# Kernel optimization log

Hardware: AMD Instinct MI355X
Metric: run time of the kernel (lower is better)

The kernel has to match this reference:

```python
import jax, jax.numpy as jnp
import numpy as np

B, D, N = 16, 512, 8192
K = 2048  # codebook_size


def setup_inputs() -> dict:
    key = jax.random.key(0)
    k1, k2 = jax.random.split(key)
    x = jax.random.normal(k1, (B, D, N), dtype=jnp.float32)
    embed = jax.random.normal(k2, (K, D), dtype=jnp.float32)  # codebook [K, D]
    return {"x": x, "embed": embed}


def reference(x, embed):
    # x: [B, D, N] -> [B, N, D] -> flatten to [B*N, D]
    xt = jnp.transpose(x, (0, 2, 1))
    flat = xt.reshape(-1, xt.shape[-1])  # [B*N, D]
    x2 = jnp.sum(flat * flat, axis=1, keepdims=True)            # [B*N, 1]
    e2 = jnp.sum(embed * embed, axis=1)[None, :]                 # [1, K]
    dist = -(x2 - 2.0 * (flat @ embed.T) + e2)                   # [B*N, K]
    embed_ind = jnp.argmax(dist, axis=-1)                        # [B*N]
    embed_ind = embed_ind.reshape(B, N)                          # [B, N]
    quantize = embed[embed_ind]                                  # [B, N, D]
    quantize = jnp.transpose(quantize, (0, 2, 1))                # [B, D, N]
    return (quantize, embed_ind)
```

## Files before the change

### kernel.cpp

```cpp
#include <hip/hip_runtime.h>
#include <math.h>
#include <stdint.h>


constexpr int B = 16, D = 512, N = 8192, K = 2048;

typedef __attribute__((ext_vector_type(8)))  short   short8;
typedef __attribute__((ext_vector_type(16))) float   floatx16;

typedef const __attribute__((address_space(1))) uint32_t* gas1_t;
typedef __attribute__((address_space(3)))       uint32_t* las3_t;

__device__ __forceinline__ void async_ld16(const void* g, void* lds) {
  __builtin_amdgcn_global_load_lds((gas1_t)g, (las3_t)lds, 16, 0, 0);
}

__device__ __forceinline__ uint32_t rne_hi(float a) {
  uint32_t u = __float_as_uint(a);
  return (u + 0x7fffu + ((u >> 16) & 1u)) & 0xffff0000u;
}

__device__ __forceinline__ void split2(float a, float b, uint32_t& hi, uint32_t& lo) {
  uint32_t ha = rne_hi(a), hb = rne_hi(b);
  float ra = a - __uint_as_float(ha);
  float rb = b - __uint_as_float(hb);
  hi = (ha >> 16) | hb;
  uint32_t la = rne_hi(ra), lb = rne_hi(rb);
  lo = (la >> 16) | lb;
}

__global__ __launch_bounds__(256) void e2_kernel(const float* __restrict__ embed,
                                                 float* __restrict__ e2) {
  int k = blockIdx.x * 4 + (threadIdx.x >> 6);
  int lane = threadIdx.x & 63;
  const float* row = embed + (size_t)k * D;
  float s = 0.f;
  #pragma unroll
  for (int d = 0; d < D; d += 64) {
    float v = row[d + lane];
    s = fmaf(v, v, s);
  }
  #pragma unroll
  for (int off = 32; off; off >>= 1) s += __shfl_down(s, off, 64);
  if (lane == 0) e2[k] = s;
}

__global__ __launch_bounds__(256) void split_x(const float* __restrict__ x,
                                               ushort* __restrict__ xhi,
                                               ushort* __restrict__ xlo) {
  const int n = blockIdx.x * 256 + threadIdx.x;
  const int g = blockIdx.y;
  const int b = blockIdx.z;
  const float* src = x + (size_t)(b * 64 + g) * 8 * N + n;
  union { ushort u[8]; short8 s; } H, L;
  #pragma unroll
  for (int r = 0; r < 8; ++r) {
    float a = src[(size_t)r * N];
    uint32_t ha = rne_hi(a);
    float ra = a - __uint_as_float(ha);
    uint32_t la = rne_hi(ra);
    H.u[r] = (ushort)(ha >> 16);
    L.u[r] = (ushort)(la >> 16);
  }
  size_t o = ((size_t)(b * 64 + g) * N + n) * 8;
  *(short8*)&xhi[o] = H.s;
  *(short8*)&xlo[o] = L.s;
}

__global__ __launch_bounds__(256) void split_e(const float* __restrict__ embed,
                                               ushort* __restrict__ ehi,
                                               ushort* __restrict__ elo) {
  const int kt = blockIdx.x, dt = blockIdx.y;
  const int t = threadIdx.x;
  const int f4 = t & 15;
  const int cr = t >> 4;
  const int run = f4 >> 1, half = f4 & 1;
  const size_t tileo = (size_t)(kt * 8 + dt) * 8192;
  const float* eb = embed + (size_t)(kt * 128) * D + dt * 64;
  #pragma unroll
  for (int p = 0; p < 8; ++p) {
    int c = p * 16 + cr;
    const float4 v = *(const float4*)(eb + (size_t)c * D + f4 * 4);
    uint32_t h0, l0, h1, l1;
    split2(v.x, v.y, h0, l0);
    split2(v.z, v.w, h1, l1);
    size_t off = tileo + (size_t)(run * 128 + c) * 8 + half * 4;
    *(uint2*)&ehi[off] = make_uint2(h0, h1);
    *(uint2*)&elo[off] = make_uint2(l0, l1);
  }
}

__global__ __launch_bounds__(256, 2) void vq_mfma2(const ushort* __restrict__ xhi,
                                                   const ushort* __restrict__ xlo,
                                                   const ushort* __restrict__ ehi,
                                                   const ushort* __restrict__ elo,
                                                   const float* __restrict__ e2g,
                                                   const float* __restrict__ embed,
                                                   float* __restrict__ out) {
  __shared__ ushort Xh[8192], Xl[8192];
  __shared__ ushort Eh[8192], El[8192];
  __shared__ float redV[512];
  __shared__ int   redI[512];
  __shared__ int   fIdx[128];

  const int t    = threadIdx.x;
  const int lane = t & 63;
  const int wid  = t >> 6;
  const int wm   = wid & 1;
  const int wn   = wid >> 1;
  const int l31  = lane & 31;
  const int lh   = lane >> 5;

  const int b  = blockIdx.y;
  const int n0 = blockIdx.x * 128;

  float bestV[2] = {-3.402823466e38f, -3.402823466e38f};
  int   bestI[2] = {0, 0};

  for (int kt = 0; kt < K / 128; ++kt) {
    floatx16 acc[2][2];
    #pragma unroll
    for (int mt = 0; mt < 2; ++mt)
      #pragma unroll
      for (int nt = 0; nt < 2; ++nt)
        #pragma unroll
        for (int i = 0; i < 16; ++i) acc[mt][nt][i] = 0.f;

    for (int dt = 0; dt < D / 64; ++dt) {
      #pragma unroll
      for (int i = 0; i < 2; ++i) {
        int gg = wid * 2 + i;
        const ushort* sh = xhi + ((size_t)(b * 64 + dt * 8 + gg) * N + n0) * 8;
        const ushort* sl = xlo + ((size_t)(b * 64 + dt * 8 + gg) * N + n0) * 8;
        #pragma unroll
        for (int j = 0; j < 2; ++j) {
          async_ld16(sh + (size_t)j * 512 + lane * 8, &Xh[gg * 1024 + j * 512]);
          async_ld16(sl + (size_t)j * 512 + lane * 8, &Xl[gg * 1024 + j * 512]);
        }
      }
      {
        const size_t tileo = (size_t)(kt * 8 + dt) * 8192;
        const ushort* sh = ehi + tileo + wid * 2048;
        const ushort* sl = elo + tileo + wid * 2048;
        #pragma unroll
        for (int i = 0; i < 4; ++i) {
          async_ld16(sh + i * 512 + lane * 8, &Eh[wid * 2048 + i * 512]);
          async_ld16(sl + i * 512 + lane * 8, &El[wid * 2048 + i * 512]);
        }
      }
      __syncthreads();

      #pragma unroll
      for (int ks = 0; ks < 4; ++ks) {
        const int run = ks * 2 + lh;
        short8 ah[2], al[2];
        #pragma unroll
        for (int mt = 0; mt < 2; ++mt) {
          int c = wm * 64 + mt * 32 + l31;
          int eo = (run * 128 + c) * 8;
          ah[mt] = *(const short8*)&Eh[eo];
          al[mt] = *(const short8*)&El[eo];
        }
        short8 bh[2], bl[2];
        #pragma unroll
        for (int nt = 0; nt < 2; ++nt) {
          int n = wn * 64 + nt * 32 + l31;
          int xo = (run * 128 + n) * 8;
          bh[nt] = *(const short8*)&Xh[xo];
          bl[nt] = *(const short8*)&Xl[xo];
        }
        #pragma unroll
        for (int mt = 0; mt < 2; ++mt)
          #pragma unroll
          for (int nt = 0; nt < 2; ++nt) {
            acc[mt][nt] = __builtin_amdgcn_mfma_f32_32x32x16_bf16(
                ah[mt], bh[nt], acc[mt][nt], 0, 0, 0);
            acc[mt][nt] = __builtin_amdgcn_mfma_f32_32x32x16_bf16(
                ah[mt], bl[nt], acc[mt][nt], 0, 0, 0);
            acc[mt][nt] = __builtin_amdgcn_mfma_f32_32x32x16_bf16(
                al[mt], bh[nt], acc[mt][nt], 0, 0, 0);
          }
      }
      __syncthreads();
    }

    #pragma unroll
    for (int mt = 0; mt < 2; ++mt) {
      #pragma unroll
      for (int r = 0; r < 16; ++r) {
        int row  = (r & 3) + 8 * (r >> 2) + 4 * lh;
        int code = kt * 128 + wm * 64 + mt * 32 + row;
        float ek = e2g[code];
        #pragma unroll
        for (int nt = 0; nt < 2; ++nt) {
          float s = 2.0f * acc[mt][nt][r] - ek;
          if (s > bestV[nt]) { bestV[nt] = s; bestI[nt] = code; }
        }
      }
    }
  }

  __syncthreads();
  #pragma unroll
  for (int nt = 0; nt < 2; ++nt) {
    int n = wn * 64 + nt * 32 + l31;
    int slot = lh + 2 * wm;
    redV[n * 4 + slot] = bestV[nt];
    redI[n * 4 + slot] = bestI[nt];
  }
  __syncthreads();
  if (t < 128) {
    float bv = redV[t * 4]; int bi = redI[t * 4];
    #pragma unroll
    for (int s = 1; s < 4; ++s) {
      float v = redV[t * 4 + s]; int ii = redI[t * 4 + s];
      if (v > bv || (v == bv && ii < bi)) { bv = v; bi = ii; }
    }
    fIdx[t] = bi;
    out[(size_t)B * D * N + (size_t)b * N + n0 + t] = (float)bi;
  }
  __syncthreads();

  {
    int n = t & 127;
    int code = fIdx[n];
    const float* erow = embed + (size_t)code * D;
    float* ob = out + (size_t)b * D * N + n0 + n;
    for (int d = (t >> 7); d < D; d += 2) {
      ob[(size_t)d * N] = erow[d];
    }
  }
}

__global__ __launch_bounds__(256, 2) void vq_mfma(const float* __restrict__ x,
                                                  const float* __restrict__ embed,
                                                  const float* __restrict__ e2g,
                                                  float* __restrict__ out) {
  __shared__ float    Xraw[64 * 128];
  __shared__ uint16_t Ehi[128 * 64];
  __shared__ uint16_t Elo[128 * 64];

  const int t    = threadIdx.x;
  const int lane = t & 63;
  const int wid  = t >> 6;
  const int wm   = wid & 1;
  const int wn   = wid >> 1;
  const int l31  = lane & 31;
  const int lh   = lane >> 5;

  const int b  = blockIdx.y;
  const int n0 = blockIdx.x * 128;
  const float* xb = x + (size_t)b * D * N + n0;

  float bestV[2] = {-3.402823466e38f, -3.402823466e38f};
  int   bestI[2] = {0, 0};

  for (int kt = 0; kt < K / 128; ++kt) {
    floatx16 acc[2][2];
    #pragma unroll
    for (int mt = 0; mt < 2; ++mt)
      #pragma unroll
      for (int nt = 0; nt < 2; ++nt)
        #pragma unroll
        for (int i = 0; i < 16; ++i) acc[mt][nt][i] = 0.f;

    for (int dt = 0; dt < D / 64; ++dt) {
      {
        const float* g0 = xb + (size_t)(dt * 64 + wid * 16 + lh) * N + l31 * 4;
        #pragma unroll
        for (int i = 0; i < 8; ++i) {
          async_ld16(g0 + (size_t)(i * 2) * N, &Xraw[(wid * 16 + i * 2) * 128]);
        }
      }
      {
        const float* eb = embed + (size_t)(kt * 128) * D + dt * 64;
        const int f4 = t & 15;
        const int cr = t >> 4;
        #pragma unroll
        for (int p = 0; p < 8; ++p) {
          int c = p * 16 + cr;
          const float4 v = *(const float4*)(eb + (size_t)c * D + f4 * 4);
          uint32_t h0, l0, h1, l1;
          split2(v.x, v.y, h0, l0);
          split2(v.z, v.w, h1, l1);
          int run = f4 >> 1, half = f4 & 1;
          int off = ((run ^ (c & 7)) * 8 + half * 4);
          *(uint2*)&Ehi[c * 64 + off] = make_uint2(h0, h1);
          *(uint2*)&Elo[c * 64 + off] = make_uint2(l0, l1);
        }
      }
      __syncthreads();

      #pragma unroll
      for (int ks = 0; ks < 4; ++ks) {
        short8 ahi[2], alo[2];
        #pragma unroll
        for (int mt = 0; mt < 2; ++mt) {
          int c = wm * 64 + mt * 32 + l31;
          int run = ks * 2 + lh;
          int off = (run ^ (c & 7)) * 8;
          ahi[mt] = *(const short8*)&Ehi[c * 64 + off];
          alo[mt] = *(const short8*)&Elo[c * 64 + off];
        }
        short8 bhi[2], blo[2];
        #pragma unroll
        for (int nt = 0; nt < 2; ++nt) {
          int n = wn * 64 + nt * 32 + l31;
          int kb = ks * 16 + lh * 8;
          float r0 = Xraw[(kb + 0) * 128 + n];
          float r1 = Xraw[(kb + 1) * 128 + n];
          float r2 = Xraw[(kb + 2) * 128 + n];
          float r3 = Xraw[(kb + 3) * 128 + n];
          float r4 = Xraw[(kb + 4) * 128 + n];
          float r5 = Xraw[(kb + 5) * 128 + n];
          float r6 = Xraw[(kb + 6) * 128 + n];
          float r7 = Xraw[(kb + 7) * 128 + n];
          union { short8 s; uint32_t u[4]; } Bh, Bl;
          split2(r0, r1, Bh.u[0], Bl.u[0]);
          split2(r2, r3, Bh.u[1], Bl.u[1]);
          split2(r4, r5, Bh.u[2], Bl.u[2]);
          split2(r6, r7, Bh.u[3], Bl.u[3]);
          bhi[nt] = Bh.s; blo[nt] = Bl.s;
        }
        #pragma unroll
        for (int mt = 0; mt < 2; ++mt)
          #pragma unroll
          for (int nt = 0; nt < 2; ++nt) {
            acc[mt][nt] = __builtin_amdgcn_mfma_f32_32x32x16_bf16(
                ahi[mt], bhi[nt], acc[mt][nt], 0, 0, 0);
            acc[mt][nt] = __builtin_amdgcn_mfma_f32_32x32x16_bf16(
                ahi[mt], blo[nt], acc[mt][nt], 0, 0, 0);
            acc[mt][nt] = __builtin_amdgcn_mfma_f32_32x32x16_bf16(
                alo[mt], bhi[nt], acc[mt][nt], 0, 0, 0);
          }
      }
      __syncthreads();
    }

    #pragma unroll
    for (int mt = 0; mt < 2; ++mt) {
      #pragma unroll
      for (int r = 0; r < 16; ++r) {
        int row  = (r & 3) + 8 * (r >> 2) + 4 * lh;
        int code = kt * 128 + wm * 64 + mt * 32 + row;
        float ek = e2g[code];
        #pragma unroll
        for (int nt = 0; nt < 2; ++nt) {
          float s = 2.0f * acc[mt][nt][r] - ek;
          if (s > bestV[nt]) { bestV[nt] = s; bestI[nt] = code; }
        }
      }
    }
  }

  __syncthreads();
  float* redV = Xraw;
  int*   redI = (int*)(Xraw + 512);
  int*   fIdx = (int*)(Xraw + 1024);

  #pragma unroll
  for (int nt = 0; nt < 2; ++nt) {
    int n = wn * 64 + nt * 32 + l31;
    int slot = lh + 2 * wm;
    redV[n * 4 + slot] = bestV[nt];
    redI[n * 4 + slot] = bestI[nt];
  }
  __syncthreads();
  if (t < 128) {
    float bv = redV[t * 4]; int bi = redI[t * 4];
    #pragma unroll
    for (int s = 1; s < 4; ++s) {
      float v = redV[t * 4 + s]; int ii = redI[t * 4 + s];
      if (v > bv || (v == bv && ii < bi)) { bv = v; bi = ii; }
    }
    fIdx[t] = bi;
    out[(size_t)B * D * N + (size_t)b * N + n0 + t] = (float)bi;
  }
  __syncthreads();

  {
    int n = t & 127;
    int code = fIdx[n];
    const float* erow = embed + (size_t)code * D;
    float* ob = out + (size_t)b * D * N + n0 + n;
    for (int d = (t >> 7); d < D; d += 2) {
      ob[(size_t)d * N] = erow[d];
    }
  }
}

extern "C" void kernel_launch(void* const* d_in, const int* in_sizes, int n_in,
                              void* d_out, int out_size, void* d_ws, size_t ws_size,
                              hipStream_t stream) {
  const float* x     = (const float*)d_in[0];
  const float* embed = (const float*)d_in[1];
  float* out = (float*)d_out;

  const size_t ES = (size_t)K * D;
  const size_t XS = (size_t)B * D * N;
  const size_t need = 8192 + 2 * ES * 2 + 2 * XS * 2;

  float* e2 = (float*)d_ws;

  if (ws_size >= need) {
    ushort* eh = (ushort*)((char*)d_ws + 8192);
    ushort* el = eh + ES;
    ushort* xh = el + ES;
    ushort* xl = xh + XS;
    e2_kernel<<<dim3(K / 4), 256, 0, stream>>>(embed, e2);
    split_e<<<dim3(K / 128, D / 64), 256, 0, stream>>>(embed, eh, el);
    split_x<<<dim3(N / 256, D / 8, B), 256, 0, stream>>>(x, xh, xl);
    vq_mfma2<<<dim3(N / 128, B), 256, 0, stream>>>(xh, xl, eh, el, e2, embed, out);
  } else {
    e2_kernel<<<dim3(K / 4), 256, 0, stream>>>(embed, e2);
    vq_mfma<<<dim3(N / 128, B), 256, 0, stream>>>(x, embed, e2, out);
  }
}
```

Before: 1.342 ms.

## Enlarge VQ MFMA tile to 256x256 with double-buffered async LDS staging

Replaces the 128x128 MFMA distance kernel with a 512-thread kernel that computes a 256-code by 256-point tile, using 32-wide d-chunks. Global-to-LDS async loads are double-buffered so the next stage's loads are issued before the current stage's MFMAs. split_x and split_e are rewritten to emit a tile-contiguous layout matching the new stages, with vectorized float4 reads in split_x. The aim is to halve operand traffic per MFMA and hide load latency. The cost is higher LDS use (about 137KB) and 128 accumulator registers, which limits occupancy to one block per CU.

```diff
diff --git a/kernel.cpp b/kernel.cpp
--- a/kernel.cpp
+++ b/kernel.cpp
@@ -46,62 +46,65 @@
 }
 
 __global__ __launch_bounds__(256) void split_x(const float* __restrict__ x,
-                                               ushort* __restrict__ xhi,
-                                               ushort* __restrict__ xlo) {
-  const int n = blockIdx.x * 256 + threadIdx.x;
-  const int g = blockIdx.y;
-  const int b = blockIdx.z;
-  const float* src = x + (size_t)(b * 64 + g) * 8 * N + n;
-  union { ushort u[8]; short8 s; } H, L;
+                                               ushort* __restrict__ xh,
+                                               ushort* __restrict__ xl) {
+  const int t  = threadIdx.x;
+  const int n0 = blockIdx.x * 1024 + t * 4;
+  const int g  = blockIdx.y;
+  const int b  = blockIdx.z;
+  const float* src = x + ((size_t)b * D + g * 8) * N + n0;
+  union { ushort u[8]; short8 s; } H[4], L[4];
   #pragma unroll
   for (int r = 0; r < 8; ++r) {
-    float a = src[(size_t)r * N];
-    uint32_t ha = rne_hi(a);
-    float ra = a - __uint_as_float(ha);
-    uint32_t la = rne_hi(ra);
-    H.u[r] = (ushort)(ha >> 16);
-    L.u[r] = (ushort)(la >> 16);
-  }
-  size_t o = ((size_t)(b * 64 + g) * N + n) * 8;
-  *(short8*)&xhi[o] = H.s;
-  *(short8*)&xlo[o] = L.s;
+    const float4 v = *(const float4*)(src + (size_t)r * N);
+    const float a0 = v.x, a1 = v.y, a2 = v.z, a3 = v.w;
+    uint32_t h; float res;
+    h = rne_hi(a0); res = a0 - __uint_as_float(h); H[0].u[r] = (ushort)(h >> 16); L[0].u[r] = (ushort)(rne_hi(res) >> 16);
+    h = rne_hi(a1); res = a1 - __uint_as_float(h); H[1].u[r] = (ushort)(h >> 16); L[1].u[r] = (ushort)(rne_hi(res) >> 16);
+    h = rne_hi(a2); res = a2 - __uint_as_float(h); H[2].u[r] = (ushort)(h >> 16); L[2].u[r] = (ushort)(rne_hi(res) >> 16);
+    h = rne_hi(a3); res = a3 - __uint_as_float(h); H[3].u[r] = (ushort)(h >> 16); L[3].u[r] = (ushort)(rne_hi(res) >> 16);
+  }
+  const size_t base = ((size_t)(b * 32 + (n0 >> 8)) * 16 + (g >> 2)) * 8192
+                    + ((size_t)(g & 3) * 256 + (n0 & 255)) * 8;
+  #pragma unroll
+  for (int j = 0; j < 4; ++j) {
+    *(short8*)&xh[base + j * 8] = H[j].s;
+    *(short8*)&xl[base + j * 8] = L[j].s;
+  }
 }
 
 __global__ __launch_bounds__(256) void split_e(const float* __restrict__ embed,
-                                               ushort* __restrict__ ehi,
-                                               ushort* __restrict__ elo) {
-  const int kt = blockIdx.x, dt = blockIdx.y;
+                                               ushort* __restrict__ eh,
+                                               ushort* __restrict__ el) {
   const int t = threadIdx.x;
-  const int f4 = t & 15;
-  const int cr = t >> 4;
-  const int run = f4 >> 1, half = f4 & 1;
-  const size_t tileo = (size_t)(kt * 8 + dt) * 8192;
-  const float* eb = embed + (size_t)(kt * 128) * D + dt * 64;
+  const int c = blockIdx.x * 16 + (t >> 4);
+  const int kt2 = c >> 8, cl = c & 255;
   #pragma unroll
   for (int p = 0; p < 8; ++p) {
-    int c = p * 16 + cr;
-    const float4 v = *(const float4*)(eb + (size_t)c * D + f4 * 4);
+    int d0 = p * 64 + (t & 15) * 4;
+    const float4 v = *(const float4*)(embed + (size_t)c * D + d0);
     uint32_t h0, l0, h1, l1;
     split2(v.x, v.y, h0, l0);
     split2(v.z, v.w, h1, l1);
-    size_t off = tileo + (size_t)(run * 128 + c) * 8 + half * 4;
-    *(uint2*)&ehi[off] = make_uint2(h0, h1);
-    *(uint2*)&elo[off] = make_uint2(l0, l1);
-  }
-}
-
-__global__ __launch_bounds__(256, 2) void vq_mfma2(const ushort* __restrict__ xhi,
-                                                   const ushort* __restrict__ xlo,
-                                                   const ushort* __restrict__ ehi,
-                                                   const ushort* __restrict__ elo,
+    int dt2 = d0 >> 5, run = (d0 >> 3) & 3, e = d0 & 7;
+    size_t off = (size_t)(kt2 * 16 + dt2) * 8192 + ((size_t)run * 256 + cl) * 8 + e;
+    *(uint2*)&eh[off] = make_uint2(h0, h1);
+    *(uint2*)&el[off] = make_uint2(l0, l1);
+  }
+}
+
+__global__ __launch_bounds__(512, 2) void vq_mfma3(const ushort* __restrict__ xh,
+                                                   const ushort* __restrict__ xl,
+                                                   const ushort* __restrict__ eh,
+                                                   const ushort* __restrict__ el,
                                                    const float* __restrict__ e2g,
                                                    const float* __restrict__ embed,
                                                    float* __restrict__ out) {
-  __shared__ ushort Xh[8192], Xl[8192];
-  __shared__ ushort Eh[8192], El[8192];
-  __shared__ float redV[512];
-  __shared__ int   redI[512];
-  __shared__ int   fIdx[128];
+  __shared__ ushort Xh[2][8192], Xl[2][8192];
+  __shared__ ushort Eh[2][8192], El[2][8192];
+  __shared__ float redV[1024];
+  __shared__ int   redI[1024];
+  __shared__ int   fIdx[256];
 
   const int t    = threadIdx.x;
   const int lane = t & 63;
@@ -112,104 +115,105 @@
   const int lh   = lane >> 5;
 
   const int b  = blockIdx.y;
-  const int n0 = blockIdx.x * 128;
+  const int nb = blockIdx.x;
+  const int n0 = nb * 256;
+
+  const size_t xbase = (size_t)(b * 32 + nb) * 16 * 8192;
 
   float bestV[2] = {-3.402823466e38f, -3.402823466e38f};
   int   bestI[2] = {0, 0};
 
-  for (int kt = 0; kt < K / 128; ++kt) {
-    floatx16 acc[2][2];
-    #pragma unroll
-    for (int mt = 0; mt < 2; ++mt)
-      #pragma unroll
-      for (int nt = 0; nt < 2; ++nt)
-        #pragma unroll
-        for (int i = 0; i < 16; ++i) acc[mt][nt][i] = 0.f;
-
-    for (int dt = 0; dt < D / 64; ++dt) {
-      #pragma unroll
-      for (int i = 0; i < 2; ++i) {
-        int gg = wid * 2 + i;
-        const ushort* sh = xhi + ((size_t)(b * 64 + dt * 8 + gg) * N + n0) * 8;
-        const ushort* sl = xlo + ((size_t)(b * 64 + dt * 8 + gg) * N + n0) * 8;
-        #pragma unroll
-        for (int j = 0; j < 2; ++j) {
-          async_ld16(sh + (size_t)j * 512 + lane * 8, &Xh[gg * 1024 + j * 512]);
-          async_ld16(sl + (size_t)j * 512 + lane * 8, &Xl[gg * 1024 + j * 512]);
-        }
-      }
-      {
-        const size_t tileo = (size_t)(kt * 8 + dt) * 8192;
-        const ushort* sh = ehi + tileo + wid * 2048;
-        const ushort* sl = elo + tileo + wid * 2048;
-        #pragma unroll
-        for (int i = 0; i < 4; ++i) {
-          async_ld16(sh + i * 512 + lane * 8, &Eh[wid * 2048 + i * 512]);
-          async_ld16(sl + i * 512 + lane * 8, &El[wid * 2048 + i * 512]);
-        }
-      }
-      __syncthreads();
-
-      #pragma unroll
-      for (int ks = 0; ks < 4; ++ks) {
-        const int run = ks * 2 + lh;
-        short8 ah[2], al[2];
-        #pragma unroll
-        for (int mt = 0; mt < 2; ++mt) {
-          int c = wm * 64 + mt * 32 + l31;
-          int eo = (run * 128 + c) * 8;
-          ah[mt] = *(const short8*)&Eh[eo];
-          al[mt] = *(const short8*)&El[eo];
-        }
-        short8 bh[2], bl[2];
+  floatx16 acc[4][2];
+  #pragma unroll
+  for (int mt = 0; mt < 4; ++mt)
+    #pragma unroll
+    for (int nt = 0; nt < 2; ++nt)
+      #pragma unroll
+      for (int i = 0; i < 16; ++i) acc[mt][nt][i] = 0.f;
+
+  auto STAGE = [&](int s, int buf) {
+    const int kt2 = s >> 4, dt2 = s & 15;
+    const size_t xo = xbase + (size_t)dt2 * 8192;
+    const size_t eo = (size_t)(kt2 * 16 + dt2) * 8192;
+    #pragma unroll
+    for (int i = 0; i < 2; ++i) {
+      const int o = (wid * 2 + i) * 512;
+      async_ld16(xh + xo + o + lane * 8, &Xh[buf][o]);
+      async_ld16(xl + xo + o + lane * 8, &Xl[buf][o]);
+      async_ld16(eh + eo + o + lane * 8, &Eh[buf][o]);
+      async_ld16(el + eo + o + lane * 8, &El[buf][o]);
+    }
+  };
+
+  STAGE(0, 0);
+  __syncthreads();
+
+  int cur = 0;
+  for (int s = 0; s < 128; ++s) {
+    if (s < 127) STAGE(s + 1, cur ^ 1);
+
+    #pragma unroll
+    for (int ks = 0; ks < 2; ++ks) {
+      const int run = ks * 2 + lh;
+      short8 ah[4], al[4];
+      #pragma unroll
+      for (int mt = 0; mt < 4; ++mt) {
+        const int eoff = (run * 256 + (wm * 128 + mt * 32 + l31)) * 8;
+        ah[mt] = *(const short8*)&Eh[cur][eoff];
+        al[mt] = *(const short8*)&El[cur][eoff];
+      }
+      short8 bh[2], bl[2];
+      #pragma unroll
+      for (int nt = 0; nt < 2; ++nt) {
+        const int xoff = (run * 256 + (wn * 64 + nt * 32 + l31)) * 8;
+        bh[nt] = *(const short8*)&Xh[cur][xoff];
+        bl[nt] = *(const short8*)&Xl[cur][xoff];
+      }
+      #pragma unroll
+      for (int mt = 0; mt < 4; ++mt)
         #pragma unroll
         for (int nt = 0; nt < 2; ++nt) {
-          int n = wn * 64 + nt * 32 + l31;
-          int xo = (run * 128 + n) * 8;
-          bh[nt] = *(const short8*)&Xh[xo];
-          bl[nt] = *(const short8*)&Xl[xo];
-        }
-        #pragma unroll
-        for (int mt = 0; mt < 2; ++mt)
+          acc[mt][nt] = __builtin_amdgcn_mfma_f32_32x32x16_bf16(
+              ah[mt], bh[nt], acc[mt][nt], 0, 0, 0);
+          acc[mt][nt] = __builtin_amdgcn_mfma_f32_32x32x16_bf16(
+              ah[mt], bl[nt], acc[mt][nt], 0, 0, 0);
+          acc[mt][nt] = __builtin_amdgcn_mfma_f32_32x32x16_bf16(
+              al[mt], bh[nt], acc[mt][nt], 0, 0, 0);
+        }
+    }
+
+    if ((s & 15) == 15) {
+      const int kt2 = s >> 4;
+      #pragma unroll
+      for (int mt = 0; mt < 4; ++mt) {
+        #pragma unroll
+        for (int r = 0; r < 16; ++r) {
+          const int row  = (r & 3) + 8 * (r >> 2) + 4 * lh;
+          const int code = kt2 * 256 + wm * 128 + mt * 32 + row;
+          const float ek = e2g[code];
           #pragma unroll
           for (int nt = 0; nt < 2; ++nt) {
-            acc[mt][nt] = __builtin_amdgcn_mfma_f32_32x32x16_bf16(
-                ah[mt], bh[nt], acc[mt][nt], 0, 0, 0);
-            acc[mt][nt] = __builtin_amdgcn_mfma_f32_32x32x16_bf16(
-                ah[mt], bl[nt], acc[mt][nt], 0, 0, 0);
-            acc[mt][nt] = __builtin_amdgcn_mfma_f32_32x32x16_bf16(
-                al[mt], bh[nt], acc[mt][nt], 0, 0, 0);
+            const float sv = 2.0f * acc[mt][nt][r] - ek;
+            if (sv > bestV[nt]) { bestV[nt] = sv; bestI[nt] = code; }
+            acc[mt][nt][r] = 0.f;
           }
-      }
-      __syncthreads();
-    }
-
-    #pragma unroll
-    for (int mt = 0; mt < 2; ++mt) {
-      #pragma unroll
-      for (int r = 0; r < 16; ++r) {
-        int row  = (r & 3) + 8 * (r >> 2) + 4 * lh;
-        int code = kt * 128 + wm * 64 + mt * 32 + row;
-        float ek = e2g[code];
-        #pragma unroll
-        for (int nt = 0; nt < 2; ++nt) {
-          float s = 2.0f * acc[mt][nt][r] - ek;
-          if (s > bestV[nt]) { bestV[nt] = s; bestI[nt] = code; }
-        }
-      }
-    }
-  }
-
-  __syncthreads();
+        }
+      }
+    }
+
+    __syncthreads();
+    cur ^= 1;
+  }
+
   #pragma unroll
   for (int nt = 0; nt < 2; ++nt) {
-    int n = wn * 64 + nt * 32 + l31;
-    int slot = lh + 2 * wm;
+    const int n = wn * 64 + nt * 32 + l31;
+    const int slot = lh * 2 + wm;
     redV[n * 4 + slot] = bestV[nt];
     redI[n * 4 + slot] = bestI[nt];
   }
   __syncthreads();
-  if (t < 128) {
+  if (t < 256) {
     float bv = redV[t * 4]; int bi = redI[t * 4];
     #pragma unroll
     for (int s = 1; s < 4; ++s) {
@@ -222,11 +226,11 @@
   __syncthreads();
 
   {
-    int n = t & 127;
-    int code = fIdx[n];
+    const int n = t & 255;
+    const int code = fIdx[n];
     const float* erow = embed + (size_t)code * D;
     float* ob = out + (size_t)b * D * N + n0 + n;
-    for (int d = (t >> 7); d < D; d += 2) {
+    for (int d = (t >> 8); d < D; d += 2) {
       ob[(size_t)d * N] = erow[d];
     }
   }
@@ -405,12 +409,12 @@
   if (ws_size >= need) {
     ushort* eh = (ushort*)((char*)d_ws + 8192);
     ushort* el = eh + ES;
-    ushort* xh = el + ES;
-    ushort* xl = xh + XS;
+    ushort* xhp = el + ES;
+    ushort* xlp = xhp + XS;
     e2_kernel<<<dim3(K / 4), 256, 0, stream>>>(embed, e2);
-    split_e<<<dim3(K / 128, D / 64), 256, 0, stream>>>(embed, eh, el);
-    split_x<<<dim3(N / 256, D / 8, B), 256, 0, stream>>>(x, xh, xl);
-    vq_mfma2<<<dim3(N / 128, B), 256, 0, stream>>>(xh, xl, eh, el, e2, embed, out);
+    split_e<<<dim3(K / 16), 256, 0, stream>>>(embed, eh, el);
+    split_x<<<dim3(N / 1024, D / 8, B), 256, 0, stream>>>(x, xhp, xlp);
+    vq_mfma3<<<dim3(N / 256, B), 512, 0, stream>>>(xhp, xlp, eh, el, e2, embed, out);
   } else {
     e2_kernel<<<dim3(K / 4), 256, 0, stream>>>(embed, e2);
     vq_mfma<<<dim3(N / 128, B), 256, 0, stream>>>(x, embed, e2, out);
```

After: 1.285 ms. 1.04x faster.
